# Optimization experiments

Hardware: AMD Instinct MI355X
Metric: run time of the kernel (lower is better)

## Reference

```python
import jax, jax.numpy as jnp
import numpy as np

NQ = 4
DIM = 2 ** NQ  # 16 basis states for the 4-qubit patch circuit


def _cnot_chain_perm():
    # Combined basis permutation for CNOT(0,1); CNOT(1,2); CNOT(2,3),
    # with wire i = bit (NQ-1-i) of the basis index (wire 0 most significant).
    idx = np.arange(DIM)
    perm = idx
    for c in range(NQ - 1):
        t = c + 1
        cbit = (idx >> (NQ - 1 - c)) & 1
        single = idx ^ (cbit << (NQ - 1 - t))  # involution: flip target iff control=1
        perm = perm[single]
    return perm

_BITS = np.array([[(b >> (NQ - 1 - i)) & 1 for i in range(NQ)] for b in range(DIM)])
CNOT_PERM = jnp.asarray(_cnot_chain_perm())
ZSIGN = jnp.asarray(1.0 - 2.0 * _BITS, dtype=jnp.float32)  # (DIM, NQ): PauliZ eigenvalues per basis/qubit


def _quantum(patches, params):
    """Exact statevector sim of: RY(x_i) -> CNOT chain -> RZ(p0) -> CNOT chain -> RZ(p1) -> <Z_i>.
    patches: (N, 4) angles; params: (2, 4). Returns (N, 4) expectation values."""
    half = 0.5 * patches
    amp = jnp.stack([jnp.cos(half), jnp.sin(half)], axis=-1)  # (N, 4, 2) per-qubit RY|0> amplitudes
    state = jnp.einsum('na,nb,nc,nd->nabcd', amp[:, 0], amp[:, 1], amp[:, 2], amp[:, 3])
    state = state.reshape(-1, DIM).astype(jnp.complex64)
    for row in range(2):
        state = state[:, CNOT_PERM]                    # CNOT chain = basis permutation
        phase = jnp.exp(-0.5j * (ZSIGN @ params[row]))  # RZ diagonal, shared across batch
        state = state * phase
    probs = jnp.real(state) ** 2 + jnp.imag(state) ** 2
    return probs @ ZSIGN  # (N, 4)


def setup_inputs() -> dict:
    key = jax.random.key(0)
    ks = jax.random.split(key, 5)
    B = 8192
    return {
        'x': jax.random.uniform(ks[0], (B, 1, 28, 28), jnp.float32),
        'params': jax.random.normal(ks[1], (2, NQ), jnp.float32),
        'W1': jax.random.normal(ks[2], (256, 784), jnp.float32) * 0.03,
        'b1': jnp.zeros((256,), jnp.float32),
        'W2': jax.random.normal(ks[3], (128, 256), jnp.float32) * 0.06,
        'b2': jnp.zeros((128,), jnp.float32),
        'W3': jax.random.normal(ks[4], (10, 128), jnp.float32) * 0.08,
        'b3': jnp.zeros((10,), jnp.float32),
    }


def reference(x, params, W1, b1, W2, b2, W3, b3):
    B = x.shape[0]
    # Extract 2x2 patches (row-major within patch, row-major patch order) -> (B*196, 4)
    patches = x[:, 0].reshape(B, 14, 2, 14, 2).transpose(0, 1, 3, 2, 4).reshape(B * 196, 4)
    feats = _quantum(patches, params).reshape(B, 196 * 4)  # cat of per-patch 4-vectors
    h = jax.nn.relu(feats @ W1.T + b1)   # Dropout is identity in eval mode
    h = jax.nn.relu(h @ W2.T + b2)
    logits = h @ W3.T + b3
    return jax.nn.log_softmax(logits, axis=-1)
```

## Files before the change

kernel.cpp:

```cpp
#include <hip/hip_runtime.h>
#include <stdint.h>

typedef __attribute__((ext_vector_type(8))) short short8;
typedef __attribute__((ext_vector_type(4))) float f32x4;

#define DEVI __device__ __forceinline__

DEVI ushort f2bf(float f) {
  union { float f; uint32_t u; } v; v.f = f;
  uint32_t r = v.u + 0x7fffu + ((v.u >> 16) & 1u);
  return (ushort)(r >> 16);
}

DEVI uint32_t cvtpk(float lo, float hi) {
  uint32_t r;
  asm("v_cvt_pk_bf16_f32 %0, %1, %2" : "=v"(r) : "v"(lo), "v"(hi));
  return r;
}
DEVI uint2 pack4(float a, float b, float c, float d) {
  uint2 o; o.x = cvtpk(a, b); o.y = cvtpk(c, d);
  return o;
}

__global__ __launch_bounds__(512) void gemm1_fused(
    const float* __restrict__ x, const float* __restrict__ W1,
    const float* __restrict__ b1, ushort* __restrict__ h1) {
  constexpr int LDA = 72;
  constexpr int NK = 13;
  __shared__ ushort As[2][64 * LDA];
  __shared__ ushort Bs[2][64 * LDA];

  const int tid = threadIdx.x;
  const int lane = tid & 63;
  const int w = tid >> 6;
  const int wm = w >> 2, wn = w & 3;
  const int bm = blockIdx.x & 127, bn = blockIdx.x >> 7;
  const int m0 = bm * 64, n0 = bn * 64;

  const int srow = tid >> 4;
  const int pl = tid & 15;
  const int kc4 = pl * 4;

  float2 atop[2], abot[2];
  float4 bw[2];

  f32x4 acc[2];
#pragma unroll
  for (int m = 0; m < 2; ++m) {
    f32x4 z = {0.f, 0.f, 0.f, 0.f};
    acc[m] = z;
  }

  auto loadT = [&](int kt) {
    const int q = kt * 16 + pl;
    if (q < 196) {
      const int i = q / 14, j = q - i * 14;
      const float* px = x + i * 56 + j * 2;
#pragma unroll
      for (int c = 0; c < 2; ++c) {
        const float* p = px + (size_t)(m0 + c * 32 + srow) * 784;
        atop[c] = *(const float2*)p;
        abot[c] = *(const float2*)(p + 28);
      }
    }
    const int k0 = kt * 64;
    if (k0 + kc4 < 784) {
#pragma unroll
      for (int c = 0; c < 2; ++c)
        bw[c] = *(const float4*)(W1 + (size_t)(n0 + c * 32 + srow) * 784 + k0 + kc4);
    } else {
#pragma unroll
      for (int c = 0; c < 2; ++c) bw[c] = make_float4(0.f, 0.f, 0.f, 0.f);
    }
  };

  auto writeT = [&](int buf, int kt) {
    const int q = kt * 16 + pl;
    ushort* as = As[buf];
    ushort* bs = Bs[buf];
    if (q < 196) {
#pragma unroll
      for (int c = 0; c < 2; ++c) {
        float c0 = __cosf(atop[c].x), c1 = __cosf(atop[c].y);
        float c2 = __cosf(abot[c].x), c3 = __cosf(abot[c].y);
        *(uint2*)(as + (c * 32 + srow) * LDA + pl * 4) =
            pack4(c0, c1, c0 * c2, c1 * c3);
      }
    } else {
      uint2 z; z.x = 0; z.y = 0;
#pragma unroll
      for (int c = 0; c < 2; ++c)
        *(uint2*)(as + (c * 32 + srow) * LDA + pl * 4) = z;
    }
#pragma unroll
    for (int c = 0; c < 2; ++c)
      *(uint2*)(bs + (c * 32 + srow) * LDA + kc4) =
          pack4(bw[c].x, bw[c].y, bw[c].z, bw[c].w);
  };

  auto mma = [&](int buf) {
    const ushort* as = As[buf];
    const ushort* bs = Bs[buf];
#pragma unroll
    for (int ks = 0; ks < 2; ++ks) {
      short8 af[2];
#pragma unroll
      for (int m = 0; m < 2; ++m) {
        int r = wm * 32 + m * 16 + (lane & 15);
        af[m] = *(const short8*)(as + r * LDA + ks * 32 + (lane >> 4) * 8);
      }
      int cdx = wn * 16 + (lane & 15);
      short8 bf = *(const short8*)(bs + cdx * LDA + ks * 32 + (lane >> 4) * 8);
#pragma unroll
      for (int m = 0; m < 2; ++m)
        acc[m] = __builtin_amdgcn_mfma_f32_16x16x32_bf16(af[m], bf, acc[m], 0, 0, 0);
    }
  };

  loadT(0);
  writeT(0, 0);
  __syncthreads();
  int cur = 0;
  for (int kt = 0; kt < NK; ++kt) {
    if (kt + 1 < NK) loadT(kt + 1);
    mma(cur);
    if (kt + 1 < NK) writeT(cur ^ 1, kt + 1);
    __syncthreads();
    cur ^= 1;
  }

#pragma unroll
  for (int m = 0; m < 2; ++m) {
    const int colg = n0 + wn * 16 + (lane & 15);
    const float bval = b1[colg];
#pragma unroll
    for (int r = 0; r < 4; ++r) {
      const int rowg = m0 + wm * 32 + m * 16 + (lane >> 4) * 4 + r;
      h1[(size_t)rowg * 256 + colg] = f2bf(fmaxf(acc[m][r] + bval, 0.f));
    }
  }
}

__global__ __launch_bounds__(256) void gemm2_head(
    const ushort* __restrict__ h1, const float* __restrict__ W2,
    const float* __restrict__ b2, const float* __restrict__ W3,
    const float* __restrict__ b3, float* __restrict__ out) {
  constexpr int LDA = 72;
  constexpr int NK = 4;
  __shared__ ushort As[2][32 * LDA];
  __shared__ ushort Bs[2][128 * LDA];
  __shared__ float h2f[32][132];
  __shared__ float W3s[1280];

  const int tid = threadIdx.x;
  const int lane = tid & 63;
  const int w = tid >> 6, wm = w >> 1, wn = w & 1;
  const int m0 = blockIdx.x * 32;

  for (int i = tid; i < 1280; i += 256) W3s[i] = W3[i];

  const int ar = tid >> 3, asl = tid & 7;
  const int br = tid >> 4, kc4 = (tid & 15) * 4;

  uint4 av;
  float4 bw[8];

  auto loadT = [&](int kt) {
    const int k0 = kt * 64;
    av = *(const uint4*)(h1 + (size_t)(m0 + ar) * 256 + k0 + asl * 8);
#pragma unroll
    for (int c = 0; c < 8; ++c)
      bw[c] = *(const float4*)(W2 + (size_t)(c * 16 + br) * 256 + k0 + kc4);
  };
  auto writeT = [&](int buf) {
    *(uint4*)(As[buf] + ar * LDA + asl * 8) = av;
#pragma unroll
    for (int c = 0; c < 8; ++c)
      *(uint2*)(Bs[buf] + (c * 16 + br) * LDA + kc4) =
          pack4(bw[c].x, bw[c].y, bw[c].z, bw[c].w);
  };

  f32x4 acc[4];
#pragma unroll
  for (int n = 0; n < 4; ++n) {
    f32x4 z = {0.f, 0.f, 0.f, 0.f};
    acc[n] = z;
  }

  auto mma = [&](int buf) {
    const ushort* as = As[buf];
    const ushort* bs = Bs[buf];
#pragma unroll
    for (int ks = 0; ks < 2; ++ks) {
      int r = wm * 16 + (lane & 15);
      short8 af = *(const short8*)(as + r * LDA + ks * 32 + (lane >> 4) * 8);
#pragma unroll
      for (int n = 0; n < 4; ++n) {
        int cdx = wn * 64 + n * 16 + (lane & 15);
        short8 bf = *(const short8*)(bs + cdx * LDA + ks * 32 + (lane >> 4) * 8);
        acc[n] = __builtin_amdgcn_mfma_f32_16x16x32_bf16(af, bf, acc[n], 0, 0, 0);
      }
    }
  };

  loadT(0);
  writeT(0);
  __syncthreads();
  int cur = 0;
  for (int kt = 0; kt < NK; ++kt) {
    if (kt + 1 < NK) loadT(kt + 1);
    mma(cur);
    if (kt + 1 < NK) writeT(cur ^ 1);
    __syncthreads();
    cur ^= 1;
  }

#pragma unroll
  for (int n = 0; n < 4; ++n) {
    int col = wn * 64 + n * 16 + (lane & 15);
    float bval = b2[col];
#pragma unroll
    for (int r = 0; r < 4; ++r)
      h2f[wm * 16 + (lane >> 4) * 4 + r][col] = fmaxf(acc[n][r] + bval, 0.f);
  }
  __syncthreads();

  {
    int r = tid >> 3, p = tid & 7;
    float a10[10];
#pragma unroll
    for (int n = 0; n < 10; ++n) a10[n] = 0.f;
#pragma unroll
    for (int e = 0; e < 16; ++e) {
      int k = e * 8 + p;
      float hv = h2f[r][k];
#pragma unroll
      for (int n = 0; n < 10; ++n) a10[n] = fmaf(hv, W3s[n * 128 + k], a10[n]);
    }
#pragma unroll
    for (int n = 0; n < 10; ++n) {
      a10[n] += __shfl_xor(a10[n], 1);
      a10[n] += __shfl_xor(a10[n], 2);
      a10[n] += __shfl_xor(a10[n], 4);
    }
    if (p == 0) {
#pragma unroll
      for (int n = 0; n < 10; ++n) a10[n] += b3[n];
      float mx = a10[0];
#pragma unroll
      for (int n = 1; n < 10; ++n) mx = fmaxf(mx, a10[n]);
      float s = 0.f;
#pragma unroll
      for (int n = 0; n < 10; ++n) s += __expf(a10[n] - mx);
      float lse = mx + __logf(s);
      float* po = out + (size_t)(m0 + r) * 10;
#pragma unroll
      for (int n = 0; n < 10; ++n) po[n] = a10[n] - lse;
    }
  }
}

extern "C" void kernel_launch(void* const* d_in, const int* in_sizes, int n_in,
                              void* d_out, int out_size, void* d_ws, size_t ws_size,
                              hipStream_t stream) {
  const float* x  = (const float*)d_in[0];
  const float* W1 = (const float*)d_in[2];
  const float* b1 = (const float*)d_in[3];
  const float* W2 = (const float*)d_in[4];
  const float* b2 = (const float*)d_in[5];
  const float* W3 = (const float*)d_in[6];
  const float* b3 = (const float*)d_in[7];
  float* out = (float*)d_out;

  ushort* h1 = (ushort*)d_ws;

  hipLaunchKernelGGL(gemm1_fused, dim3(512), dim3(512), 0, stream, x, W1, b1, h1);
  hipLaunchKernelGGL(gemm2_head, dim3(256), dim3(256), 0, stream, h1, W2, b2, W3, b3, out);
}
```

Baseline: 28.18 us.

## Halve gemm2 row tile and widen blocks to 512 threads for more parallelism

The second GEMM plus head kernel now processes 16 rows per block instead of 32, with 8 waves each owning a 16-column slice of the 128 outputs, and launches 512 blocks. This aims to fill more compute units and shorten each block's serial chain. In exchange, W2 is reloaded and converted twice as often in total, and the head reduction uses a wider shuffle tree.

```diff
diff --git a/kernel.cpp b/kernel.cpp
--- a/kernel.cpp
+++ b/kernel.cpp
@@ -141,65 +141,62 @@
   }
 }
 
-__global__ __launch_bounds__(256) void gemm2_head(
+__global__ __launch_bounds__(512) void gemm2_head(
     const ushort* __restrict__ h1, const float* __restrict__ W2,
     const float* __restrict__ b2, const float* __restrict__ W3,
     const float* __restrict__ b3, float* __restrict__ out) {
   constexpr int LDA = 72;
   constexpr int NK = 4;
-  __shared__ ushort As[2][32 * LDA];
+  __shared__ ushort As[2][16 * LDA];
   __shared__ ushort Bs[2][128 * LDA];
-  __shared__ float h2f[32][132];
+  __shared__ float h2f[16][132];
   __shared__ float W3s[1280];
 
   const int tid = threadIdx.x;
   const int lane = tid & 63;
-  const int w = tid >> 6, wm = w >> 1, wn = w & 1;
-  const int m0 = blockIdx.x * 32;
-
-  for (int i = tid; i < 1280; i += 256) W3s[i] = W3[i];
-
+  const int w = tid >> 6;
+  const int m0 = blockIdx.x * 16;
+
+  for (int i = tid; i < 1280; i += 512) W3s[i] = W3[i];
+
+  const bool ldA = tid < 128;
   const int ar = tid >> 3, asl = tid & 7;
-  const int br = tid >> 4, kc4 = (tid & 15) * 4;
 
   uint4 av;
-  float4 bw[8];
+  float4 bw[4];
 
   auto loadT = [&](int kt) {
     const int k0 = kt * 64;
-    av = *(const uint4*)(h1 + (size_t)(m0 + ar) * 256 + k0 + asl * 8);
-#pragma unroll
-    for (int c = 0; c < 8; ++c)
-      bw[c] = *(const float4*)(W2 + (size_t)(c * 16 + br) * 256 + k0 + kc4);
+    if (ldA) av = *(const uint4*)(h1 + (size_t)(m0 + ar) * 256 + k0 + asl * 8);
+#pragma unroll
+    for (int c = 0; c < 4; ++c) {
+      const int flat = c * 512 + tid, r = flat >> 4, sl = flat & 15;
+      bw[c] = *(const float4*)(W2 + (size_t)r * 256 + k0 + sl * 4);
+    }
   };
   auto writeT = [&](int buf) {
-    *(uint4*)(As[buf] + ar * LDA + asl * 8) = av;
-#pragma unroll
-    for (int c = 0; c < 8; ++c)
-      *(uint2*)(Bs[buf] + (c * 16 + br) * LDA + kc4) =
+    if (ldA) *(uint4*)(As[buf] + ar * LDA + asl * 8) = av;
+#pragma unroll
+    for (int c = 0; c < 4; ++c) {
+      const int flat = c * 512 + tid, r = flat >> 4, sl = flat & 15;
+      *(uint2*)(Bs[buf] + r * LDA + sl * 4) =
           pack4(bw[c].x, bw[c].y, bw[c].z, bw[c].w);
-  };
-
-  f32x4 acc[4];
-#pragma unroll
-  for (int n = 0; n < 4; ++n) {
+    }
+  };
+
+  f32x4 acc;
+  {
     f32x4 z = {0.f, 0.f, 0.f, 0.f};
-    acc[n] = z;
+    acc = z;
   }
 
   auto mma = [&](int buf) {
-    const ushort* as = As[buf];
-    const ushort* bs = Bs[buf];
 #pragma unroll
     for (int ks = 0; ks < 2; ++ks) {
-      int r = wm * 16 + (lane & 15);
-      short8 af = *(const short8*)(as + r * LDA + ks * 32 + (lane >> 4) * 8);
-#pragma unroll
-      for (int n = 0; n < 4; ++n) {
-        int cdx = wn * 64 + n * 16 + (lane & 15);
-        short8 bf = *(const short8*)(bs + cdx * LDA + ks * 32 + (lane >> 4) * 8);
-        acc[n] = __builtin_amdgcn_mfma_f32_16x16x32_bf16(af, bf, acc[n], 0, 0, 0);
-      }
+      short8 af = *(const short8*)(As[buf] + (lane & 15) * LDA + ks * 32 + (lane >> 4) * 8);
+      const int cdx = w * 16 + (lane & 15);
+      short8 bf = *(const short8*)(Bs[buf] + cdx * LDA + ks * 32 + (lane >> 4) * 8);
+      acc = __builtin_amdgcn_mfma_f32_16x16x32_bf16(af, bf, acc, 0, 0, 0);
     }
   };
 
@@ -207,6 +204,7 @@
   writeT(0);
   __syncthreads();
   int cur = 0;
+#pragma unroll
   for (int kt = 0; kt < NK; ++kt) {
     if (kt + 1 < NK) loadT(kt + 1);
     mma(cur);
@@ -215,25 +213,24 @@
     cur ^= 1;
   }
 
-#pragma unroll
-  for (int n = 0; n < 4; ++n) {
-    int col = wn * 64 + n * 16 + (lane & 15);
-    float bval = b2[col];
+  {
+    const int col = w * 16 + (lane & 15);
+    const float bval = b2[col];
 #pragma unroll
     for (int r = 0; r < 4; ++r)
-      h2f[wm * 16 + (lane >> 4) * 4 + r][col] = fmaxf(acc[n][r] + bval, 0.f);
+      h2f[(lane >> 4) * 4 + r][col] = fmaxf(acc[r] + bval, 0.f);
   }
   __syncthreads();
 
   {
-    int r = tid >> 3, p = tid & 7;
+    const int r = tid >> 5, p = tid & 31;
     float a10[10];
 #pragma unroll
     for (int n = 0; n < 10; ++n) a10[n] = 0.f;
 #pragma unroll
-    for (int e = 0; e < 16; ++e) {
-      int k = e * 8 + p;
-      float hv = h2f[r][k];
+    for (int e = 0; e < 4; ++e) {
+      const int k = e * 32 + p;
+      const float hv = h2f[r][k];
 #pragma unroll
       for (int n = 0; n < 10; ++n) a10[n] = fmaf(hv, W3s[n * 128 + k], a10[n]);
     }
@@ -242,6 +239,8 @@
       a10[n] += __shfl_xor(a10[n], 1);
       a10[n] += __shfl_xor(a10[n], 2);
       a10[n] += __shfl_xor(a10[n], 4);
+      a10[n] += __shfl_xor(a10[n], 8);
+      a10[n] += __shfl_xor(a10[n], 16);
     }
     if (p == 0) {
 #pragma unroll
@@ -252,7 +251,7 @@
       float s = 0.f;
 #pragma unroll
       for (int n = 0; n < 10; ++n) s += __expf(a10[n] - mx);
-      float lse = mx + __logf(s);
+      const float lse = mx + __logf(s);
       float* po = out + (size_t)(m0 + r) * 10;
 #pragma unroll
       for (int n = 0; n < 10; ++n) po[n] = a10[n] - lse;
@@ -275,5 +274,5 @@
   ushort* h1 = (ushort*)d_ws;
 
   hipLaunchKernelGGL(gemm1_fused, dim3(512), dim3(512), 0, stream, x, W1, b1, h1);
-  hipLaunchKernelGGL(gemm2_head, dim3(256), dim3(256), 0, stream, h1, W2, b2, W3, b3, out);
-}
+  hipLaunchKernelGGL(gemm2_head, dim3(512), dim3(512), 0, stream, h1, W2, b2, W3, b3, out);
+}
```

Result: slower. 28.92 us (+2.6%).
